# Kernel tuning notes

Measured on AMD Instinct MI355X. Metric: run time of the kernel, lower is better.

## Reference

```python
import jax, jax.numpy as jnp
import numpy as np

N, E, IN_DIM, HID, HEADS = 50000, 800000, 128, 16, 8
EPS_BN = 1e-5


def _gat_conv(x, edge_index, W, att_src, att_dst, bias, heads, out_ch, concat):
    # x: [N, F_in]; W: [heads*out_ch, F_in]; att_*: [heads, out_ch]
    n = x.shape[0]
    h = (x @ W.T).reshape(n, heads, out_ch)            # [N, H, C]
    a_src = (h * att_src[None]).sum(-1)                # [N, H]
    a_dst = (h * att_dst[None]).sum(-1)                # [N, H]
    src, dst = edge_index[0], edge_index[1]
    alpha = jax.nn.leaky_relu(a_src[src] + a_dst[dst], negative_slope=0.2)  # [E, H]
    # segment softmax over destination node (per head)
    amax = jax.ops.segment_max(alpha, dst, num_segments=n)
    amax = jnp.where(jnp.isfinite(amax), amax, 0.0)
    ex = jnp.exp(alpha - amax[dst])
    denom = jax.ops.segment_sum(ex, dst, num_segments=n)
    attn = ex / (denom[dst] + 1e-16)                   # [E, H]
    msg = h[src] * attn[:, :, None]                    # [E, H, C]
    out = jax.ops.segment_sum(msg, dst, num_segments=n)  # [N, H, C]
    out = out.reshape(n, heads * out_ch) if concat else out.mean(axis=1)
    return out + bias


def _bn_eval(h, mean, var, gamma, beta):
    return (h - mean) * jax.lax.rsqrt(var + EPS_BN) * gamma + beta


def setup_inputs() -> dict:
    key = jax.random.key(0)
    ks = jax.random.split(key, 16)
    s = 0.1
    inp = {
        "x": jax.random.normal(ks[0], (N, IN_DIM), jnp.float32),
        "edge_index": jax.random.randint(ks[1], (2, E), 0, N, jnp.int32),
        # layer 0: GATConv(128 -> 16, heads=8, concat)
        "w0": jax.random.normal(ks[2], (HEADS * HID, IN_DIM), jnp.float32) * s,
        "asrc0": jax.random.normal(ks[3], (HEADS, HID), jnp.float32) * s,
        "adst0": jax.random.normal(ks[4], (HEADS, HID), jnp.float32) * s,
        "b0": jnp.zeros((HEADS * HID,), jnp.float32),
        "skip0": jax.random.normal(ks[5], (HEADS * HID, IN_DIM), jnp.float32) * s,
        "bn0_g": jnp.ones((HEADS * HID,), jnp.float32),
        "bn0_b": jnp.zeros((HEADS * HID,), jnp.float32),
        "bn0_m": jax.random.normal(ks[6], (HEADS * HID,), jnp.float32) * s,
        "bn0_v": jax.random.uniform(ks[7], (HEADS * HID,), jnp.float32, 0.5, 1.5),
        # layer 1: GATConv(128 -> 16, heads=1, concat=False)
        "w1": jax.random.normal(ks[8], (HID, HEADS * HID), jnp.float32) * s,
        "asrc1": jax.random.normal(ks[9], (1, HID), jnp.float32) * s,
        "adst1": jax.random.normal(ks[10], (1, HID), jnp.float32) * s,
        "b1": jnp.zeros((HID,), jnp.float32),
        "skip1": jax.random.normal(ks[11], (HID, HEADS * HID), jnp.float32) * s,
        "bn1_g": jnp.ones((HID,), jnp.float32),
        "bn1_b": jnp.zeros((HID,), jnp.float32),
        "bn1_m": jax.random.normal(ks[12], (HID,), jnp.float32) * s,
        "bn1_v": jax.random.uniform(ks[13], (HID,), jnp.float32, 0.5, 1.5),
    }
    return inp


def reference(x, edge_index, w0, asrc0, adst0, b0, skip0, bn0_g, bn0_b, bn0_m, bn0_v,
              w1, asrc1, adst1, b1, skip1, bn1_g, bn1_b, bn1_m, bn1_v):
    # eval mode: dropout = identity, BN uses running stats
    h_in = x
    h = _gat_conv(h_in, edge_index, w0, asrc0, adst0, b0, HEADS, HID, True)   # [N, 128]
    h = _bn_eval(h, bn0_m, bn0_v, bn0_g, bn0_b)
    h = h + h_in @ skip0.T
    h = jax.nn.elu(h)
    h_in = h
    h = _gat_conv(h_in, edge_index, w1, asrc1, adst1, b1, 1, HID, False)      # [N, 16]
    h = _bn_eval(h, bn1_m, bn1_v, bn1_g, bn1_b)
    h = h + h_in @ skip1.T
    h = jax.nn.elu(h)
    return h
```

## Files before the change

### kernel.cpp

```cpp
#include <hip/hip_runtime.h>
#include <hip/hip_bf16.h>

#define NN 50000
#define EE 800000
#define INDIM 128
#define HIDC 16
#define NHEAD 8
#define COARSE 196
#define EPB 2048
#define CAPR 6144
#define CAPB 8192
#define CVT_BLKS 37
#define AGG0_BLKS 2048

typedef __attribute__((ext_vector_type(8))) short bf16x8;
typedef __attribute__((ext_vector_type(4))) float f32x4;
typedef __attribute__((ext_vector_type(2))) float f32x2;

#if defined(__has_builtin)
#if __has_builtin(__builtin_amdgcn_cvt_pk_f32_fp8)
#define HAVE_PK_F32_FP8 1
#endif
#endif

__device__ __forceinline__ float bf2f(unsigned short u) {
    union { float f; unsigned int i; } v; v.i = ((unsigned int)u) << 16; return v.f;
}
__device__ __forceinline__ unsigned short f2bf(float f) {
    union { float f; unsigned int i; } v; v.f = f;
    unsigned int r = v.i + 0x7FFFu + ((v.i >> 16) & 1u);
    return (unsigned short)(r >> 16);
}

__global__ __launch_bounds__(256) void k_prep(
    const float* __restrict__ w0, const float* __restrict__ skip0,
    const float* __restrict__ w1, const float* __restrict__ skip1,
    const float* __restrict__ b0, const float* __restrict__ g0,
    const float* __restrict__ bb0, const float* __restrict__ m0,
    const float* __restrict__ v0,
    const float* __restrict__ b1, const float* __restrict__ g1,
    const float* __restrict__ bb1, const float* __restrict__ m1,
    const float* __restrict__ v1,
    unsigned int* __restrict__ wb2, unsigned int* __restrict__ wb1_2,
    float2* __restrict__ acb0, float2* __restrict__ acb1,
    const int* __restrict__ ei, int* __restrict__ ccur0,
    unsigned int* __restrict__ pairs)
{
    if (blockIdx.x < CVT_BLKS) {
        const long NW = 256 * 128 / 4;
        const long NW1 = 32 * 128 / 4;
        long i = (long)blockIdx.x * 256 + threadIdx.x;
        if (i < NW) {
            const float4* src = (i < 128 * 128 / 4) ? ((const float4*)w0 + i)
                                                    : ((const float4*)skip0 + (i - 128 * 128 / 4));
            float4 v = *src;
            wb2[i * 2]     = (unsigned int)f2bf(v.x) | ((unsigned int)f2bf(v.y) << 16);
            wb2[i * 2 + 1] = (unsigned int)f2bf(v.z) | ((unsigned int)f2bf(v.w) << 16);
        } else if (i < NW + NW1) {
            long j = i - NW;
            const float4* src = (j < 16 * 128 / 4) ? ((const float4*)w1 + j)
                                                   : ((const float4*)skip1 + (j - 16 * 128 / 4));
            float4 v = *src;
            wb1_2[j * 2]     = (unsigned int)f2bf(v.x) | ((unsigned int)f2bf(v.y) << 16);
            wb1_2[j * 2 + 1] = (unsigned int)f2bf(v.z) | ((unsigned int)f2bf(v.w) << 16);
        } else if (i < NW + NW1 + 128) {
            int c = (int)(i - NW - NW1);
            float A = g0[c] * rsqrtf(v0[c] + 1e-5f);
            acb0[c] = make_float2(A, (b0[c] - m0[c]) * A + bb0[c]);
        } else if (i < NW + NW1 + 128 + 16) {
            int c = (int)(i - NW - NW1 - 128);
            float A = g1[c] * rsqrtf(v1[c] + 1e-5f);
            acb1[c] = make_float2(A, (b1[c] - m1[c]) * A + bb1[c]);
        }
        return;
    }

    __shared__ int bcnt[256];
    __shared__ int lofs[256];
    __shared__ int gofs[256];
    __shared__ unsigned int stage[EPB];
    __shared__ int gpos[EPB];
    const int t = threadIdx.x;
    const int e0 = (blockIdx.x - CVT_BLKS) * EPB;

    bcnt[t] = 0;
    __syncthreads();

    int mybin[8], myrank[8];
    unsigned int mypair[8];
    #pragma unroll
    for (int k = 0; k < 8; k++) {
        int e = e0 + k * 256 + t;
        mybin[k] = -1;
        if (e < EE) {
            int s = ei[e], d = ei[EE + e];
            int b = d >> 8;
            myrank[k] = atomicAdd(&bcnt[b], 1);
            mybin[k] = b;
            mypair[k] = ((unsigned)d << 16) | (unsigned)s;
        }
    }
    __syncthreads();

    int v = bcnt[t];
    lofs[t] = v;
    __syncthreads();
    for (int off = 1; off < 256; off <<= 1) {
        int u = (t >= off) ? lofs[t - off] : 0;
        __syncthreads();
        lofs[t] += u;
        __syncthreads();
    }
    if (t < COARSE && v > 0)
        gofs[t] = t * CAPR + atomicAdd(&ccur0[t], v);
    __syncthreads();

    #pragma unroll
    for (int k = 0; k < 8; k++) {
        int b = mybin[k];
        if (b >= 0) {
            int slot = (lofs[b] - bcnt[b]) + myrank[k];
            stage[slot] = mypair[k];
            gpos[slot]  = gofs[b] + myrank[k];
        }
    }
    __syncthreads();

    const int total = lofs[255];
    for (int i = t; i < total; i += 256)
        pairs[gpos[i]] = stage[i];
}

__global__ __launch_bounds__(256) void k_mid(
    const unsigned int* __restrict__ pairs, const int* __restrict__ ccur0,
    unsigned short* __restrict__ srcidx, int* __restrict__ rowbeg,
    int* __restrict__ deg,
    const float* __restrict__ x, const unsigned short* __restrict__ wb,
    const float* __restrict__ asrc0, const float* __restrict__ adst0,
    unsigned char* __restrict__ h0f, unsigned short* __restrict__ s0b,
    float* __restrict__ a_src0, float* __restrict__ a_dst0)
{
    __shared__ int fcnt[256], fofs[256], fcur[256];
    __shared__ unsigned short stage[CAPB];

    if (blockIdx.x < COARSE) {
        const int b = blockIdx.x, t = threadIdx.x;
        const int beg = b * CAPR;
        int cnt = ccur0[b];
        if (cnt > CAPR) cnt = CAPR;

        fcnt[t] = 0;
        __syncthreads();
        for (int i = t; i < cnt; i += 256) {
            unsigned int d = pairs[beg + i] >> 16;
            atomicAdd(&fcnt[d & 255], 1);
        }
        __syncthreads();

        int v = fcnt[t];
        fofs[t] = v;
        __syncthreads();
        for (int off = 1; off < 256; off <<= 1) {
            int u = (t >= off) ? fofs[t - off] : 0;
            __syncthreads();
            fofs[t] += u;
            __syncthreads();
        }
        int ex = fofs[t] - v;
        int node = b * 256 + t;
        if (node < NN) { rowbeg[node] = beg + ex; deg[node] = v; }
        fcur[t] = ex;
        __syncthreads();

        for (int i = t; i < cnt; i += 256) {
            unsigned int p = pairs[beg + i];
            unsigned int d = p >> 16;
            int slot = atomicAdd(&fcur[d & 255], 1);
            stage[slot] = (unsigned short)(p & 0xFFFFu);
        }
        __syncthreads();
        for (int i = t; i < cnt; i += 256)
            srcidx[beg + i] = stage[i];
        return;
    }

    const int bid = blockIdx.x - COARSE;
    const int wave = threadIdx.x >> 6;
    const int lane = threadIdx.x & 63;
    const int lrow = lane & 15;
    const int quad = lane >> 4;
    const int rowbase = bid * 32;

    bf16x8 afrag[2][4];
    #pragma unroll
    for (int sub = 0; sub < 2; sub++) {
        const int row = min(rowbase + sub * 16 + lrow, NN - 1);
        const float* xr = x + (long)row * 128;
        #pragma unroll
        for (int ki = 0; ki < 4; ki++) {
            float4 a = *(const float4*)(xr + ki * 32 + quad * 8);
            float4 b = *(const float4*)(xr + ki * 32 + quad * 8 + 4);
            bf16x8 f;
            f[0] = (short)f2bf(a.x); f[1] = (short)f2bf(a.y);
            f[2] = (short)f2bf(a.z); f[3] = (short)f2bf(a.w);
            f[4] = (short)f2bf(b.x); f[5] = (short)f2bf(b.y);
            f[6] = (short)f2bf(b.z); f[7] = (short)f2bf(b.w);
            afrag[sub][ki] = f;
        }
    }

    #pragma unroll
    for (int t = 0; t < 4; t++) {
        const int jg = wave * 64 + t * 16 + lrow;
        bf16x8 bfrag[4];
        #pragma unroll
        for (int ki = 0; ki < 4; ki++)
            bfrag[ki] = *(const bf16x8*)(wb + (long)jg * 128 + ki * 32 + quad * 8);
        float4 asv = {0.f, 0.f, 0.f, 0.f}, adv = {0.f, 0.f, 0.f, 0.f};
        if (wave < 2) {
            const int cb = wave * 64 + t * 16 + quad * 4;
            asv = *(const float4*)(asrc0 + cb);
            adv = *(const float4*)(adst0 + cb);
        }
        #pragma unroll
        for (int sub = 0; sub < 2; sub++) {
            f32x4 acc = (f32x4){0.f, 0.f, 0.f, 0.f};
            #pragma unroll
            for (int ki = 0; ki < 4; ki++)
                acc = __builtin_amdgcn_mfma_f32_16x16x32_bf16(bfrag[ki], afrag[sub][ki], acc, 0, 0, 0);

            const int node = rowbase + sub * 16 + lrow;
            if (node < NN) {
                if (wave < 2) {
                    const int cb = wave * 64 + t * 16 + quad * 4;
                    unsigned int u = __builtin_amdgcn_cvt_pk_fp8_f32(acc[0], acc[1], 0u, 0);
                    u = __builtin_amdgcn_cvt_pk_fp8_f32(acc[2], acc[3], u, 1);
                    *(unsigned int*)(h0f + (long)node * 128 + cb) = u;
                    float ps = acc[0] * asv.x + acc[1] * asv.y + acc[2] * asv.z + acc[3] * asv.w;
                    float pd = acc[0] * adv.x + acc[1] * adv.y + acc[2] * adv.z + acc[3] * adv.w;
                    ps += __shfl_xor(ps, 16); ps += __shfl_xor(ps, 32);
                    pd += __shfl_xor(pd, 16); pd += __shfl_xor(pd, 32);
                    if (quad == 0) {
                        const int h = wave * 4 + t;
                        a_src0[(long)node * 8 + h] = ps;
                        a_dst0[(long)node * 8 + h] = pd;
                    }
                } else {
                    const int cb = (wave - 2) * 64 + t * 16 + quad * 4;
                    uint2 u;
                    u.x = (unsigned int)f2bf(acc[0]) | ((unsigned int)f2bf(acc[1]) << 16);
                    u.y = (unsigned int)f2bf(acc[2]) | ((unsigned int)f2bf(acc[3]) << 16);
                    *(uint2*)(s0b + (long)node * 128 + cb) = u;
                }
            }
        }
    }
}

__global__ __launch_bounds__(256) void k_agg0(
    const int* __restrict__ rowbeg, const int* __restrict__ deg,
    const unsigned short* __restrict__ srcidx,
    const unsigned char* __restrict__ h0f, const float* __restrict__ a_src0,
    const float* __restrict__ a_dst0, const unsigned short* __restrict__ s0b,
    const float2* __restrict__ acb0, unsigned short* __restrict__ hab)
{
    const int wid = (blockIdx.x * 256 + threadIdx.x) >> 6;
    const int nwaves = AGG0_BLKS * 4;
    const int lane = threadIdx.x & 63;
    const int eslot = lane >> 3;
    const int hph1 = lane & 7;
    const int l16 = lane & 15;
    const int c0 = l16 * 8;
    const int hsel = l16 >> 1;
    const int q = lane >> 4;

    for (int d = wid; d < NN; d += nwaves) {
        const int beg = rowbeg[d], end = beg + deg[d];
        const float adst = a_dst0[d * 8 + hph1];

        float den = 0.f;
        f32x2 acc2[4] = {(f32x2){0.f, 0.f}, (f32x2){0.f, 0.f},
                         (f32x2){0.f, 0.f}, (f32x2){0.f, 0.f}};
        for (int i = beg; i < end; i += 16) {
            const int idxA = i + eslot;
            const int idxB = i + 8 + eslot;
            const bool vA = idxA < end;
            const bool vB = idxB < end;
            const int sA = vA ? (int)srcidx[idxA] : 0;
            const int sB = vB ? (int)srcidx[idxB] : 0;
            float aA = a_src0[sA * 8 + hph1] + adst;
            float aB = a_src0[sB * 8 + hph1] + adst;
            aA = aA > 0.f ? aA : 0.2f * aA;
            aB = aB > 0.f ? aB : 0.2f * aB;
            const float wA = vA ? __expf(aA) : 0.f;
            const float wB = vB ? __expf(aB) : 0.f;
            den += wA + wB;
            #pragma unroll
            for (int kk = 0; kk < 2; kk++) {
                const int k8 = (kk * 4 + q) * 8;
                const float wa = __shfl(wA, k8 + hsel);
                const int   sa = __shfl(sA, k8);
                const float wb = __shfl(wB, k8 + hsel);
                const int   sb = __shfl(sB, k8);
                const uint2 ua = *(const uint2*)(h0f + ((unsigned)sa << 7) + c0);
                const uint2 ub = *(const uint2*)(h0f + ((unsigned)sb << 7) + c0);
#ifdef HAVE_PK_F32_FP8
                f32x2 pa0 = __builtin_amdgcn_cvt_pk_f32_fp8((int)ua.x, false);
                f32x2 pa1 = __builtin_amdgcn_cvt_pk_f32_fp8((int)ua.x, true);
                f32x2 pa2 = __builtin_amdgcn_cvt_pk_f32_fp8((int)ua.y, false);
                f32x2 pa3 = __builtin_amdgcn_cvt_pk_f32_fp8((int)ua.y, true);
                f32x2 pb0 = __builtin_amdgcn_cvt_pk_f32_fp8((int)ub.x, false);
                f32x2 pb1 = __builtin_amdgcn_cvt_pk_f32_fp8((int)ub.x, true);
                f32x2 pb2 = __builtin_amdgcn_cvt_pk_f32_fp8((int)ub.y, false);
                f32x2 pb3 = __builtin_amdgcn_cvt_pk_f32_fp8((int)ub.y, true);
                acc2[0] += wa * pa0 + wb * pb0;
                acc2[1] += wa * pa1 + wb * pb1;
                acc2[2] += wa * pa2 + wb * pb2;
                acc2[3] += wa * pa3 + wb * pb3;
#else
                acc2[0][0] += wa * __builtin_amdgcn_cvt_f32_fp8(ua.x, 0)
                            + wb * __builtin_amdgcn_cvt_f32_fp8(ub.x, 0);
                acc2[0][1] += wa * __builtin_amdgcn_cvt_f32_fp8(ua.x, 1)
                            + wb * __builtin_amdgcn_cvt_f32_fp8(ub.x, 1);
                acc2[1][0] += wa * __builtin_amdgcn_cvt_f32_fp8(ua.x, 2)
                            + wb * __builtin_amdgcn_cvt_f32_fp8(ub.x, 2);
                acc2[1][1] += wa * __builtin_amdgcn_cvt_f32_fp8(ua.x, 3)
                            + wb * __builtin_amdgcn_cvt_f32_fp8(ub.x, 3);
                acc2[2][0] += wa * __builtin_amdgcn_cvt_f32_fp8(ua.y, 0)
                            + wb * __builtin_amdgcn_cvt_f32_fp8(ub.y, 0);
                acc2[2][1] += wa * __builtin_amdgcn_cvt_f32_fp8(ua.y, 1)
                            + wb * __builtin_amdgcn_cvt_f32_fp8(ub.y, 1);
                acc2[3][0] += wa * __builtin_amdgcn_cvt_f32_fp8(ua.y, 2)
                            + wb * __builtin_amdgcn_cvt_f32_fp8(ub.y, 2);
                acc2[3][1] += wa * __builtin_amdgcn_cvt_f32_fp8(ua.y, 3)
                            + wb * __builtin_amdgcn_cvt_f32_fp8(ub.y, 3);
#endif
            }
        }
        den += __shfl_xor(den, 8);
        den += __shfl_xor(den, 16);
        den += __shfl_xor(den, 32);
        const float denh = __shfl(den, hsel);
        #pragma unroll
        for (int p = 0; p < 4; p++) {
            acc2[p][0] += __shfl_xor(acc2[p][0], 16);
            acc2[p][0] += __shfl_xor(acc2[p][0], 32);
            acc2[p][1] += __shfl_xor(acc2[p][1], 16);
            acc2[p][1] += __shfl_xor(acc2[p][1], 32);
        }

        if (q == 0) {
            const float inv = 1.f / (denh + 1e-16f);
            const float4* abf = (const float4*)((const float*)acb0 + 2 * c0);
            const uint4 su = *(const uint4*)(s0b + (long)d * 128 + c0);
            const unsigned int sw[4] = {su.x, su.y, su.z, su.w};
            unsigned int res[4];
            #pragma unroll
            for (int p = 0; p < 4; p++) {
                const float4 ab = abf[p];
                float x0 = acc2[p][0] * inv * ab.x + ab.y + bf2f((unsigned short)sw[p]);
                float x1 = acc2[p][1] * inv * ab.z + ab.w + bf2f((unsigned short)(sw[p] >> 16));
                x0 = x0 > 0.f ? x0 : __expf(x0) - 1.f;
                x1 = x1 > 0.f ? x1 : __expf(x1) - 1.f;
                res[p] = (unsigned int)f2bf(x0) | ((unsigned int)f2bf(x1) << 16);
            }
            *(uint4*)(hab + (long)d * 128 + c0) = make_uint4(res[0], res[1], res[2], res[3]);
        }
    }
}

__global__ __launch_bounds__(256) void k_post0(
    const unsigned short* __restrict__ hab,
    const unsigned short* __restrict__ wb1,
    const float* __restrict__ asrc1, const float* __restrict__ adst1,
    unsigned short* __restrict__ h1b, float* __restrict__ s1,
    float* __restrict__ a_src1, float* __restrict__ a_dst1)
{
    const int tid = threadIdx.x;
    const int lane = tid & 63, wave = tid >> 6;
    const int lrow = lane & 15, quad = lane >> 4;

    bf16x8 bfrag[2][4];
    #pragma unroll
    for (int t = 0; t < 2; t++)
        #pragma unroll
        for (int ki = 0; ki < 4; ki++)
            bfrag[t][ki] = *(const bf16x8*)(wb1 + (long)(t * 16 + lrow) * 128 + ki * 32 + quad * 8);
    const float avec = asrc1[lrow];
    const float dvec = adst1[lrow];

    const int tile = blockIdx.x * 4 + wave;
    if (tile * 16 >= NN) return;
    const int n0 = tile * 16;
    const long arow = (long)(n0 + lrow) * 128;

    bf16x8 afrag[4];
    #pragma unroll
    for (int ki = 0; ki < 4; ki++)
        afrag[ki] = *(const bf16x8*)(hab + arow + ki * 32 + quad * 8);

    f32x4 acc0 = (f32x4){0.f, 0.f, 0.f, 0.f};
    f32x4 acc1 = (f32x4){0.f, 0.f, 0.f, 0.f};
    #pragma unroll
    for (int ki = 0; ki < 4; ki++) {
        acc0 = __builtin_amdgcn_mfma_f32_16x16x32_bf16(afrag[ki], bfrag[0][ki], acc0, 0, 0, 0);
        acc1 = __builtin_amdgcn_mfma_f32_16x16x32_bf16(afrag[ki], bfrag[1][ki], acc1, 0, 0, 0);
    }

    #pragma unroll
    for (int r = 0; r < 4; r++) {
        const int node = n0 + quad * 4 + r;
        h1b[(long)node * 16 + lrow] = f2bf(acc0[r]);
        s1[(long)node * 16 + lrow] = acc1[r];
        float ps = acc0[r] * avec;
        float pd = acc0[r] * dvec;
        ps += __shfl_xor(ps, 1); ps += __shfl_xor(ps, 2);
        ps += __shfl_xor(ps, 4); ps += __shfl_xor(ps, 8);
        pd += __shfl_xor(pd, 1); pd += __shfl_xor(pd, 2);
        pd += __shfl_xor(pd, 4); pd += __shfl_xor(pd, 8);
        if (lrow == 0) { a_src1[node] = ps; a_dst1[node] = pd; }
    }
}

__global__ __launch_bounds__(256) void k_agg1_final(
    const int* __restrict__ rowbeg, const int* __restrict__ deg,
    const unsigned short* __restrict__ srcidx,
    const unsigned short* __restrict__ h1b, const float* __restrict__ a_src1,
    const float* __restrict__ a_dst1, const float* __restrict__ s1,
    const float2* __restrict__ acb1, float* __restrict__ out)
{
    const int gid = blockIdx.x * 256 + threadIdx.x;
    const int d = gid >> 3;
    if (d >= NN) return;
    const int lane = threadIdx.x & 63;
    const int gl = lane & 7;
    const int gb = lane & ~7;
    const int c0 = (gl & 1) * 8;
    const int q = gl >> 1;
    const int beg = rowbeg[d], end = beg + deg[d];
    const float adst = a_dst1[d];

    float den = 0.f;
    float acc[8] = {0.f, 0.f, 0.f, 0.f, 0.f, 0.f, 0.f, 0.f};
    for (int i = beg; i < end; i += 16) {
        const int idxA = i + gl;
        const int idxB = i + 8 + gl;
        const bool vA = idxA < end;
        const bool vB = idxB < end;
        const int sA = vA ? (int)srcidx[idxA] : 0;
        const int sB = vB ? (int)srcidx[idxB] : 0;
        float aA = a_src1[sA] + adst;
        float aB = a_src1[sB] + adst;
        aA = aA > 0.f ? aA : 0.2f * aA;
        aB = aB > 0.f ? aB : 0.2f * aB;
        const float wA = vA ? __expf(aA) : 0.f;
        const float wB = vB ? __expf(aB) : 0.f;
        den += wA + wB;
        #pragma unroll
        for (int kk = 0; kk < 2; kk++) {
            const int k = kk * 4 + q;
            const float wa = __shfl(wA, gb | k);
            const int   sa = __shfl(sA, gb | k);
            const float wb = __shfl(wB, gb | k);
            const int   sb = __shfl(sB, gb | k);
            const uint4 ua = *(const uint4*)(h1b + sa * 16 + c0);
            const uint4 ub = *(const uint4*)(h1b + sb * 16 + c0);
            const unsigned int uw[8] = {ua.x, ua.y, ua.z, ua.w, ub.x, ub.y, ub.z, ub.w};
            #pragma unroll
            for (int p = 0; p < 4; p++) {
                acc[2 * p]     += wa * bf2f((unsigned short)uw[p]);
                acc[2 * p + 1] += wa * bf2f((unsigned short)(uw[p] >> 16));
                acc[2 * p]     += wb * bf2f((unsigned short)uw[p + 4]);
                acc[2 * p + 1] += wb * bf2f((unsigned short)(uw[p + 4] >> 16));
            }
        }
    }
    den += __shfl_xor(den, 1);
    den += __shfl_xor(den, 2);
    den += __shfl_xor(den, 4);
    #pragma unroll
    for (int p = 0; p < 8; p++) {
        acc[p] += __shfl_xor(acc[p], 2);
        acc[p] += __shfl_xor(acc[p], 4);
    }

    if (q == 0) {
        const float inv = 1.f / (den + 1e-16f);
        const float4* abf = (const float4*)((const float*)acb1 + 2 * c0);
        const float4 sv0 = *(const float4*)(s1 + (long)d * 16 + c0);
        const float4 sv1 = *(const float4*)(s1 + (long)d * 16 + c0 + 4);
        const float svf[8] = {sv0.x, sv0.y, sv0.z, sv0.w, sv1.x, sv1.y, sv1.z, sv1.w};
        float o[8];
        #pragma unroll
        for (int p = 0; p < 4; p++) {
            const float4 ab = abf[p];
            float v0o = acc[2 * p]     * inv * ab.x + ab.y + svf[2 * p];
            float v1o = acc[2 * p + 1] * inv * ab.z + ab.w + svf[2 * p + 1];
            o[2 * p]     = v0o > 0.f ? v0o : __expf(v0o) - 1.f;
            o[2 * p + 1] = v1o > 0.f ? v1o : __expf(v1o) - 1.f;
        }
        *(float4*)(out + (long)d * 16 + c0)     = make_float4(o[0], o[1], o[2], o[3]);
        *(float4*)(out + (long)d * 16 + c0 + 4) = make_float4(o[4], o[5], o[6], o[7]);
    }
}

extern "C" void kernel_launch(void* const* d_in, const int* in_sizes, int n_in,
                              void* d_out, int out_size, void* d_ws, size_t ws_size,
                              hipStream_t stream)
{
    (void)in_sizes; (void)n_in; (void)out_size; (void)ws_size;
    const float* x     = (const float*)d_in[0];
    const int*   ei    = (const int*)d_in[1];
    const float* w0    = (const float*)d_in[2];
    const float* asrc0 = (const float*)d_in[3];
    const float* adst0 = (const float*)d_in[4];
    const float* b0    = (const float*)d_in[5];
    const float* skip0 = (const float*)d_in[6];
    const float* bn0g  = (const float*)d_in[7];
    const float* bn0b  = (const float*)d_in[8];
    const float* bn0m  = (const float*)d_in[9];
    const float* bn0v  = (const float*)d_in[10];
    const float* w1    = (const float*)d_in[11];
    const float* asrc1 = (const float*)d_in[12];
    const float* adst1 = (const float*)d_in[13];
    const float* b1    = (const float*)d_in[14];
    const float* skip1 = (const float*)d_in[15];
    const float* bn1g  = (const float*)d_in[16];
    const float* bn1b  = (const float*)d_in[17];
    const float* bn1m  = (const float*)d_in[18];
    const float* bn1v  = (const float*)d_in[19];

    const long NPAIR = (long)COARSE * CAPR;
    unsigned int* pairs = (unsigned int*)d_ws;
    unsigned short* wb    = (unsigned short*)(pairs + NPAIR);
    unsigned short* wb1   = wb + 256 * 128;
    unsigned short* s0b   = wb1 + 32 * 128;
    unsigned short* hab   = s0b + (long)NN * 128;
    unsigned short* h1b   = hab + (long)NN * 128;
    unsigned short* srcidx= h1b + (long)NN * 16;
    unsigned char*  h0f   = (unsigned char*)(srcidx + NPAIR);
    float* a_src0 = (float*)(h0f + (long)NN * 128);
    float* a_dst0 = a_src0 + (long)NN * 8;
    float* s1     = a_dst0 + (long)NN * 8;
    float* a_src1 = s1 + (long)NN * 16;
    float* a_dst1 = a_src1 + NN;
    float2* acb0  = (float2*)(a_dst1 + NN);
    float2* acb1  = acb0 + 128;
    int* ccur0  = (int*)(acb1 + 16);
    int* rowbeg = ccur0 + COARSE;
    int* deg    = rowbeg + NN;

    hipMemsetAsync(ccur0, 0, (size_t)COARSE * 4, stream);

    const int PREP_BLKS = CVT_BLKS + (EE + EPB - 1) / EPB;
    k_prep<<<PREP_BLKS, 256, 0, stream>>>(
        w0, skip0, w1, skip1,
        b0, bn0g, bn0b, bn0m, bn0v, b1, bn1g, bn1b, bn1m, bn1v,
        (unsigned int*)wb, (unsigned int*)wb1, acb0, acb1,
        ei, ccur0, pairs);

    const int MID_BLKS = COARSE + (NN + 31) / 32;
    k_mid<<<MID_BLKS, 256, 0, stream>>>(
        pairs, ccur0, srcidx, rowbeg, deg,
        x, wb, asrc0, adst0, h0f, s0b, a_src0, a_dst0);

    k_agg0<<<AGG0_BLKS, 256, 0, stream>>>(rowbeg, deg, srcidx, h0f,
                                          a_src0, a_dst0, s0b, acb0,
                                          hab);
    k_post0<<<(NN / 16 + 3) / 4, 256, 0, stream>>>(hab, wb1, asrc1, adst1,
                                                   h1b, s1, a_src1, a_dst1);
    k_agg1_final<<<(NN * 8 + 255) / 256, 256, 0, stream>>>(rowbeg, deg, srcidx, h1b,
                                                           a_src1, a_dst1, s1,
                                                           acb1, (float*)d_out);
}
```

Baseline: 209.1 us.

## Split layer-0 aggregation into two head-half passes with per-lane edge ownership

```diff
diff --git a/kernel.cpp b/kernel.cpp
--- a/kernel.cpp
+++ b/kernel.cpp
@@ -268,103 +268,75 @@
     const int nwaves = AGG0_BLKS * 4;
     const int lane = threadIdx.x & 63;
     const int eslot = lane >> 3;
-    const int hph1 = lane & 7;
-    const int l16 = lane & 15;
-    const int c0 = l16 * 8;
-    const int hsel = l16 >> 1;
-    const int q = lane >> 4;
-
-    for (int d = wid; d < NN; d += nwaves) {
-        const int beg = rowbeg[d], end = beg + deg[d];
-        const float adst = a_dst0[d * 8 + hph1];
-
-        float den = 0.f;
-        f32x2 acc2[4] = {(f32x2){0.f, 0.f}, (f32x2){0.f, 0.f},
-                         (f32x2){0.f, 0.f}, (f32x2){0.f, 0.f}};
-        for (int i = beg; i < end; i += 16) {
-            const int idxA = i + eslot;
-            const int idxB = i + 8 + eslot;
-            const bool vA = idxA < end;
-            const bool vB = idxB < end;
-            const int sA = vA ? (int)srcidx[idxA] : 0;
-            const int sB = vB ? (int)srcidx[idxB] : 0;
-            float aA = a_src0[sA * 8 + hph1] + adst;
-            float aB = a_src0[sB * 8 + hph1] + adst;
-            aA = aA > 0.f ? aA : 0.2f * aA;
-            aB = aB > 0.f ? aB : 0.2f * aB;
-            const float wA = vA ? __expf(aA) : 0.f;
-            const float wB = vB ? __expf(aB) : 0.f;
-            den += wA + wB;
-            #pragma unroll
-            for (int kk = 0; kk < 2; kk++) {
-                const int k8 = (kk * 4 + q) * 8;
-                const float wa = __shfl(wA, k8 + hsel);
-                const int   sa = __shfl(sA, k8);
-                const float wb = __shfl(wB, k8 + hsel);
-                const int   sb = __shfl(sB, k8);
-                const uint2 ua = *(const uint2*)(h0f + ((unsigned)sa << 7) + c0);
-                const uint2 ub = *(const uint2*)(h0f + ((unsigned)sb << 7) + c0);
+    const int cg = lane & 7;
+    const int hoff = cg >> 1;
+
+    #pragma unroll
+    for (int pass = 0; pass < 2; pass++) {
+        const int h = pass * 4 + hoff;
+        const int c0 = pass * 64 + cg * 8;
+        for (int d = wid; d < NN; d += nwaves) {
+            const int beg = rowbeg[d], end = beg + deg[d];
+            const float adst = a_dst0[d * 8 + h];
+
+            float den = 0.f;
+            f32x2 acc[4] = {(f32x2){0.f, 0.f}, (f32x2){0.f, 0.f},
+                            (f32x2){0.f, 0.f}, (f32x2){0.f, 0.f}};
+            for (int i = beg; i < end; i += 8) {
+                const int e = i + eslot;
+                const bool v = e < end;
+                const int s = v ? (int)srcidx[e] : 0;
+                float a = a_src0[s * 8 + h] + adst;
+                a = a > 0.f ? a : 0.2f * a;
+                const float w = v ? __expf(a) : 0.f;
+                den += w;
+                const uint2 u = *(const uint2*)(h0f + ((unsigned)s << 7) + c0);
 #ifdef HAVE_PK_F32_FP8
-                f32x2 pa0 = __builtin_amdgcn_cvt_pk_f32_fp8((int)ua.x, false);
-                f32x2 pa1 = __builtin_amdgcn_cvt_pk_f32_fp8((int)ua.x, true);
-                f32x2 pa2 = __builtin_amdgcn_cvt_pk_f32_fp8((int)ua.y, false);
-                f32x2 pa3 = __builtin_amdgcn_cvt_pk_f32_fp8((int)ua.y, true);
-                f32x2 pb0 = __builtin_amdgcn_cvt_pk_f32_fp8((int)ub.x, false);
-                f32x2 pb1 = __builtin_amdgcn_cvt_pk_f32_fp8((int)ub.x, true);
-                f32x2 pb2 = __builtin_amdgcn_cvt_pk_f32_fp8((int)ub.y, false);
-                f32x2 pb3 = __builtin_amdgcn_cvt_pk_f32_fp8((int)ub.y, true);
-                acc2[0] += wa * pa0 + wb * pb0;
-                acc2[1] += wa * pa1 + wb * pb1;
-                acc2[2] += wa * pa2 + wb * pb2;
-                acc2[3] += wa * pa3 + wb * pb3;
+                acc[0] += w * __builtin_amdgcn_cvt_pk_f32_fp8((int)u.x, false);
+                acc[1] += w * __builtin_amdgcn_cvt_pk_f32_fp8((int)u.x, true);
+                acc[2] += w * __builtin_amdgcn_cvt_pk_f32_fp8((int)u.y, false);
+                acc[3] += w * __builtin_amdgcn_cvt_pk_f32_fp8((int)u.y, true);
 #else
-                acc2[0][0] += wa * __builtin_amdgcn_cvt_f32_fp8(ua.x, 0)
-                            + wb * __builtin_amdgcn_cvt_f32_fp8(ub.x, 0);
-                acc2[0][1] += wa * __builtin_amdgcn_cvt_f32_fp8(ua.x, 1)
-                            + wb * __builtin_amdgcn_cvt_f32_fp8(ub.x, 1);
-                acc2[1][0] += wa * __builtin_amdgcn_cvt_f32_fp8(ua.x, 2)
-                            + wb * __builtin_amdgcn_cvt_f32_fp8(ub.x, 2);
-                acc2[1][1] += wa * __builtin_amdgcn_cvt_f32_fp8(ua.x, 3)
-                            + wb * __builtin_amdgcn_cvt_f32_fp8(ub.x, 3);
-                acc2[2][0] += wa * __builtin_amdgcn_cvt_f32_fp8(ua.y, 0)
-                            + wb * __builtin_amdgcn_cvt_f32_fp8(ub.y, 0);
-                acc2[2][1] += wa * __builtin_amdgcn_cvt_f32_fp8(ua.y, 1)
-                            + wb * __builtin_amdgcn_cvt_f32_fp8(ub.y, 1);
-                acc2[3][0] += wa * __builtin_amdgcn_cvt_f32_fp8(ua.y, 2)
-                            + wb * __builtin_amdgcn_cvt_f32_fp8(ub.y, 2);
-                acc2[3][1] += wa * __builtin_amdgcn_cvt_f32_fp8(ua.y, 3)
-                            + wb * __builtin_amdgcn_cvt_f32_fp8(ub.y, 3);
+                acc[0][0] += w * __builtin_amdgcn_cvt_f32_fp8(u.x, 0);
+                acc[0][1] += w * __builtin_amdgcn_cvt_f32_fp8(u.x, 1);
+                acc[1][0] += w * __builtin_amdgcn_cvt_f32_fp8(u.x, 2);
+                acc[1][1] += w * __builtin_amdgcn_cvt_f32_fp8(u.x, 3);
+                acc[2][0] += w * __builtin_amdgcn_cvt_f32_fp8(u.y, 0);
+                acc[2][1] += w * __builtin_amdgcn_cvt_f32_fp8(u.y, 1);
+                acc[3][0] += w * __builtin_amdgcn_cvt_f32_fp8(u.y, 2);
+                acc[3][1] += w * __builtin_amdgcn_cvt_f32_fp8(u.y, 3);
 #endif
             }
-        }
-        den += __shfl_xor(den, 8);
-        den += __shfl_xor(den, 16);
-        den += __shfl_xor(den, 32);
-        const float denh = __shfl(den, hsel);
-        #pragma unroll
-        for (int p = 0; p < 4; p++) {
-            acc2[p][0] += __shfl_xor(acc2[p][0], 16);
-            acc2[p][0] += __shfl_xor(acc2[p][0], 32);
-            acc2[p][1] += __shfl_xor(acc2[p][1], 16);
-            acc2[p][1] += __shfl_xor(acc2[p][1], 32);
-        }
-
-        if (q == 0) {
-            const float inv = 1.f / (denh + 1e-16f);
-            const float4* abf = (const float4*)((const float*)acb0 + 2 * c0);
-            const uint4 su = *(const uint4*)(s0b + (long)d * 128 + c0);
-            const unsigned int sw[4] = {su.x, su.y, su.z, su.w};
-            unsigned int res[4];
+            den += __shfl_xor(den, 8);
+            den += __shfl_xor(den, 16);
+            den += __shfl_xor(den, 32);
             #pragma unroll
             for (int p = 0; p < 4; p++) {
-                const float4 ab = abf[p];
-                float x0 = acc2[p][0] * inv * ab.x + ab.y + bf2f((unsigned short)sw[p]);
-                float x1 = acc2[p][1] * inv * ab.z + ab.w + bf2f((unsigned short)(sw[p] >> 16));
-                x0 = x0 > 0.f ? x0 : __expf(x0) - 1.f;
-                x1 = x1 > 0.f ? x1 : __expf(x1) - 1.f;
-                res[p] = (unsigned int)f2bf(x0) | ((unsigned int)f2bf(x1) << 16);
+                acc[p][0] += __shfl_xor(acc[p][0], 8);
+                acc[p][0] += __shfl_xor(acc[p][0], 16);
+                acc[p][0] += __shfl_xor(acc[p][0], 32);
+                acc[p][1] += __shfl_xor(acc[p][1], 8);
+                acc[p][1] += __shfl_xor(acc[p][1], 16);
+                acc[p][1] += __shfl_xor(acc[p][1], 32);
             }
-            *(uint4*)(hab + (long)d * 128 + c0) = make_uint4(res[0], res[1], res[2], res[3]);
+
+            if (eslot == 0) {
+                const float inv = 1.f / (den + 1e-16f);
+                const float4* abf = (const float4*)((const float*)acb0 + 2 * c0);
+                const uint4 su = *(const uint4*)(s0b + (long)d * 128 + c0);
+                const unsigned int sw[4] = {su.x, su.y, su.z, su.w};
+                unsigned int res[4];
+                #pragma unroll
+                for (int p = 0; p < 4; p++) {
+                    const float4 ab = abf[p];
+                    float x0 = acc[p][0] * inv * ab.x + ab.y + bf2f((unsigned short)sw[p]);
+                    float x1 = acc[p][1] * inv * ab.z + ab.w + bf2f((unsigned short)(sw[p] >> 16));
+                    x0 = x0 > 0.f ? x0 : __expf(x0) - 1.f;
+                    x1 = x1 > 0.f ? x1 : __expf(x1) - 1.f;
+                    res[p] = (unsigned int)f2bf(x0) | ((unsigned int)f2bf(x1) << 16);
+                }
+                *(uint4*)(hab + (long)d * 128 + c0) = make_uint4(res[0], res[1], res[2], res[3]);
+            }
         }
     }
 }
```

New measurement: 233.7 us. 11.8% more time.
